# Optimization experiments

Hardware: AMD Instinct MI355X
Metric: run time of the kernel (lower is better)

## Reference

```python
import jax, jax.numpy as jnp
import numpy as np

N_NODES = 50000
N_EDGES = 800000
IN_DIM = 256
HID = 64          # per-head hidden dim
HEADS = 4
OUT_DIM = 64
NEG_SLOPE = 0.2


def setup_inputs() -> dict:
    key = jax.random.key(0)
    ks = jax.random.split(key, 10)
    x = jax.random.normal(ks[0], (N_NODES, IN_DIM), dtype=jnp.float32)
    src = jax.random.randint(ks[1], (N_EDGES,), 0, N_NODES, dtype=jnp.int32)
    dst = jax.random.randint(ks[2], (N_EDGES,), 0, N_NODES, dtype=jnp.int32)
    # layer 1: IN_DIM -> HEADS x HID (concat)
    W1 = jax.random.normal(ks[3], (IN_DIM, HEADS * HID), dtype=jnp.float32) * (1.0 / np.sqrt(IN_DIM))
    al1 = jax.random.normal(ks[4], (HEADS, HID), dtype=jnp.float32) * 0.1
    ar1 = jax.random.normal(ks[5], (HEADS, HID), dtype=jnp.float32) * 0.1
    W2 = jax.random.normal(ks[6], (HEADS * HID, 1 * OUT_DIM), dtype=jnp.float32) * (1.0 / np.sqrt(HEADS * HID))
    al2 = jax.random.normal(ks[7], (1, OUT_DIM), dtype=jnp.float32) * 0.1
    ar2 = jax.random.normal(ks[8], (1, OUT_DIM), dtype=jnp.float32) * 0.1
    return {"x": x, "src": src, "dst": dst, "W1": W1, "al1": al1, "ar1": ar1,
            "W2": W2, "al2": al2, "ar2": ar2}


def gat_layer(h, src, dst, W, al, ar):
    # h: [N, F_in]; W: [F_in, H*D]; al/ar: [H, D]
    H, D = al.shape
    feat = (h @ W).reshape(-1, H, D)                       # [N, H, D]
    el = jnp.einsum('nhd,hd->nh', feat, al)                # [N, H]
    er = jnp.einsum('nhd,hd->nh', feat, ar)                # [N, H]
    e = jax.nn.leaky_relu(el[src] + er[dst], negative_slope=NEG_SLOPE)  # [E, H]
    # softmax over incoming edges of each destination node
    m = jax.ops.segment_max(e, dst, num_segments=N_NODES)  # [N, H]
    w = jnp.exp(e - m[dst])                                # [E, H]
    s = jax.ops.segment_sum(w, dst, num_segments=N_NODES)  # [N, H]
    alpha = w / s[dst]                                     # [E, H]
    msg = feat[src] * alpha[:, :, None]                    # [E, H, D]
    out = jax.ops.segment_sum(msg, dst, num_segments=N_NODES)  # [N, H, D]
    return out


def reference(x, src, dst, W1, al1, ar1, W2, al2, ar2):
    # layer 1: concat heads + elu (dropout disabled: eval mode)
    h1 = gat_layer(x, src, dst, W1, al1, ar1)              # [N, HEADS, HID]
    h1 = jax.nn.elu(h1.reshape(N_NODES, HEADS * HID))      # [N, HEADS*HID]
    # output layer: single head, mean over heads (trivial for H=1)
    h2 = gat_layer(h1, src, dst, W2, al2, ar2)             # [N, 1, OUT_DIM]
    logits = h2.mean(axis=1)                               # [N, OUT_DIM]
    return logits
```

## Files before the change

kernel.cpp:

```cpp
#include <hip/hip_runtime.h>
#include <math.h>

#define NNODES 50000
#define NEDGES 800000
#define INDIM 256
#define HID 64
#define HEADS 4
#define OUTDIM 64
#define NEG_SLOPE 0.2f
#define NB ((NNODES + 1023) / 1024)
#define HB ((NEDGES + 255) / 256)
#define XB ((NNODES * (INDIM / 8) + 255) / 256)
#define WB ((256 * 256 + 256 * 64 + 255) / 256)

typedef __attribute__((ext_vector_type(4))) float f32x4;
typedef _Float16 __attribute__((ext_vector_type(8))) half8;


__global__ __launch_bounds__(256) void bsum_kernel(const int* __restrict__ deg,
                                                   int* __restrict__ bsums) {
    int b = blockIdx.x, t = threadIdx.x;
    int base = b * 1024 + t * 4;
    int s = 0;
    #pragma unroll
    for (int e = 0; e < 4; ++e) { int i = base + e; if (i < NNODES) s += deg[i]; }
    #pragma unroll
    for (int o = 32; o; o >>= 1) s += __shfl_xor(s, o);
    __shared__ int ws[4];
    int lane = t & 63, wid = t >> 6;
    if (lane == 0) ws[wid] = s;
    __syncthreads();
    if (t == 0) bsums[b] = ws[0] + ws[1] + ws[2] + ws[3];
}

__global__ __launch_bounds__(256) void scan_write_kernel(const int* __restrict__ deg,
                                                         const int* __restrict__ bsums,
                                                         int* __restrict__ offs) {
    int b = blockIdx.x, t = threadIdx.x;
    int lane = t & 63, wid = t >> 6;
    int bv = (lane < b) ? bsums[lane] : 0;
    #pragma unroll
    for (int o = 32; o; o >>= 1) bv += __shfl_xor(bv, o);
    int base = b * 1024 + t * 4;
    int v[4]; int tsum = 0;
    #pragma unroll
    for (int e = 0; e < 4; ++e) {
        int i = base + e;
        v[e] = (i < NNODES) ? deg[i] : 0;
        tsum += v[e];
    }
    int p = tsum;
    #pragma unroll
    for (int o = 1; o < 64; o <<= 1) { int u = __shfl_up(p, o); if (lane >= o) p += u; }
    __shared__ int ws[4];
    if (lane == 63) ws[wid] = p;
    __syncthreads();
    int woff = 0;
    for (int i = 0; i < wid; ++i) woff += ws[i];
    int run = bv + woff + p - tsum;
    #pragma unroll
    for (int e = 0; e < 4; ++e) {
        int i = base + e;
        if (i < NNODES) { offs[i] = run; run += v[e]; }
    }
    if (b == 0 && t == 0) offs[NNODES] = NEDGES;
}


__global__ __launch_bounds__(256) void prep_kernel(const int* __restrict__ dst,
                                                   int* __restrict__ deg,
                                                   int* __restrict__ rank,
                                                   const float* __restrict__ W1,
                                                   _Float16* __restrict__ W1t,
                                                   const float* __restrict__ W2,
                                                   _Float16* __restrict__ W2t,
                                                   const float* __restrict__ x,
                                                   _Float16* __restrict__ xh) {
    int b = blockIdx.x;
    if (b < HB) {
        int i = b * 256 + threadIdx.x;
        if (i < NEDGES) rank[i] = atomicAdd(&deg[dst[i]], 1);
    } else if (b < HB + XB) {
        int i = (b - HB) * 256 + threadIdx.x;
        if (i < NNODES * (INDIM / 8)) {
            const float4* xp = (const float4*)x;
            float4 f0 = xp[(size_t)i * 2];
            float4 f1 = xp[(size_t)i * 2 + 1];
            half8 v;
            v[0] = (_Float16)f0.x; v[1] = (_Float16)f0.y;
            v[2] = (_Float16)f0.z; v[3] = (_Float16)f0.w;
            v[4] = (_Float16)f1.x; v[5] = (_Float16)f1.y;
            v[6] = (_Float16)f1.z; v[7] = (_Float16)f1.w;
            ((half8*)xh)[i] = v;
        }
    } else {
        int idx = (b - HB - XB) * 256 + threadIdx.x;
        if (idx < 256 * 256) {
            int k = idx >> 8, n = idx & 255;
            W1t[n * 256 + k] = (_Float16)W1[idx];
        } else if (idx < 256 * 256 + 256 * 64) {
            int j = idx - 256 * 256;
            int k = j >> 6, n = j & 63;
            W2t[n * 256 + k] = (_Float16)W2[j];
        }
    }
}


template <int BM, int BN, int ELR>
__device__ __forceinline__ void gemm_body(
        const _Float16* __restrict__ Ah,
        const _Float16* __restrict__ Bt,
        _Float16* __restrict__ C,
        const float* __restrict__ al, const float* __restrict__ ar,
        float* __restrict__ el, float* __restrict__ er,
        int M, int N, int m0, int n0) {
    constexpr int K = 256;
    constexpr int NT = BN / 32;
    constexpr int TM = BM / 32;
    int t = threadIdx.x;
    int lane = t & 63, w = t >> 6;
    int wm = w >> 1, wn = w & 1;
    int lr = lane & 15, quad = lane >> 4;

    f32x4 acc[TM][NT];
    #pragma unroll
    for (int i = 0; i < TM; ++i)
        #pragma unroll
        for (int j = 0; j < NT; ++j) acc[i][j] = (f32x4){0.f, 0.f, 0.f, 0.f};

    int arow[TM];
    #pragma unroll
    for (int i = 0; i < TM; ++i) {
        int r = m0 + wm * (BM / 2) + i * 16 + lr;
        arow[i] = (r < M) ? r : (M - 1);
    }
    int brow[NT];
    #pragma unroll
    for (int j = 0; j < NT; ++j) brow[j] = n0 + wn * NT * 16 + j * 16 + lr;

    #pragma unroll
    for (int kk = 0; kk < K; kk += 32) {
        half8 a[TM], b[NT];
        #pragma unroll
        for (int i = 0; i < TM; ++i)
            a[i] = *(const half8*)(Ah + (size_t)arow[i] * K + kk + quad * 8);
        #pragma unroll
        for (int j = 0; j < NT; ++j)
            b[j] = *(const half8*)(Bt + (size_t)brow[j] * K + kk + quad * 8);
        #pragma unroll
        for (int i = 0; i < TM; ++i)
            #pragma unroll
            for (int j = 0; j < NT; ++j)
                acc[i][j] = __builtin_amdgcn_mfma_f32_16x16x32_f16(a[i], b[j], acc[i][j], 0, 0, 0);
    }
    #pragma unroll
    for (int i = 0; i < TM; ++i) {
        #pragma unroll
        for (int r = 0; r < 4; ++r) {
            int row = m0 + wm * (BM / 2) + i * 16 + quad * 4 + r;
            if (row < M) {
                #pragma unroll
                for (int j = 0; j < NT; ++j)
                    C[(size_t)row * N + n0 + wn * NT * 16 + j * 16 + lr] =
                        (_Float16)acc[i][j][r];
            }
        }
    }
    if constexpr (ELR == 1) {
        int h = n0 / 64 + wn;
        float alh[NT], arh[NT];
        #pragma unroll
        for (int j = 0; j < NT; ++j) {
            alh[j] = al[h * 64 + j * 16 + lr];
            arh[j] = ar[h * 64 + j * 16 + lr];
        }
        #pragma unroll
        for (int i = 0; i < TM; ++i) {
            #pragma unroll
            for (int r = 0; r < 4; ++r) {
                float pel = 0.f, per = 0.f;
                #pragma unroll
                for (int j = 0; j < NT; ++j) {
                    pel = fmaf(acc[i][j][r], alh[j], pel);
                    per = fmaf(acc[i][j][r], arh[j], per);
                }
                #pragma unroll
                for (int o = 1; o < 16; o <<= 1) {
                    pel += __shfl_xor(pel, o);
                    per += __shfl_xor(per, o);
                }
                if (lr == 0) {
                    int row = m0 + wm * (BM / 2) + i * 16 + quad * 4 + r;
                    if (row < M) {
                        el[(size_t)row * 4 + h] = pel;
                        er[(size_t)row * 4 + h] = per;
                    }
                }
            }
        }
    }
    if constexpr (ELR == 2) {
        __shared__ float elbuf[BM], erbuf[BM];
        float alv[NT], arv[NT];
        #pragma unroll
        for (int j = 0; j < NT; ++j) {
            alv[j] = al[wn * NT * 16 + j * 16 + lr];
            arv[j] = ar[wn * NT * 16 + j * 16 + lr];
        }
        float pel_s[TM][4], per_s[TM][4];
        #pragma unroll
        for (int i = 0; i < TM; ++i) {
            #pragma unroll
            for (int r = 0; r < 4; ++r) {
                float pel = 0.f, per = 0.f;
                #pragma unroll
                for (int j = 0; j < NT; ++j) {
                    pel = fmaf(acc[i][j][r], alv[j], pel);
                    per = fmaf(acc[i][j][r], arv[j], per);
                }
                #pragma unroll
                for (int o = 1; o < 16; o <<= 1) {
                    pel += __shfl_xor(pel, o);
                    per += __shfl_xor(per, o);
                }
                pel_s[i][r] = pel; per_s[i][r] = per;
            }
        }
        if (wn == 1 && lr == 0) {
            #pragma unroll
            for (int i = 0; i < TM; ++i)
                #pragma unroll
                for (int r = 0; r < 4; ++r) {
                    int rl = wm * (BM / 2) + i * 16 + quad * 4 + r;
                    elbuf[rl] = pel_s[i][r];
                    erbuf[rl] = per_s[i][r];
                }
        }
        __syncthreads();
        if (wn == 0 && lr == 0) {
            #pragma unroll
            for (int i = 0; i < TM; ++i)
                #pragma unroll
                for (int r = 0; r < 4; ++r) {
                    int rl = wm * (BM / 2) + i * 16 + quad * 4 + r;
                    int row = m0 + rl;
                    if (row < M) {
                        el[row] = pel_s[i][r] + elbuf[rl];
                        er[row] = per_s[i][r] + erbuf[rl];
                    }
                }
        }
    }
}


__global__ __launch_bounds__(256) void gemm1_scatter_kernel(
        const _Float16* __restrict__ Ah, const _Float16* __restrict__ Bt,
        _Float16* __restrict__ C,
        const float* __restrict__ al, const float* __restrict__ ar,
        float* __restrict__ el, float* __restrict__ er,
        int gemmBlocks,
        const int* __restrict__ src, const int* __restrict__ dst,
        const int* __restrict__ rank,
        const int* __restrict__ offs,
        int* __restrict__ ssorted) {
    int b = blockIdx.x;
    if (b < gemmBlocks) {
        int m0 = (b >> 1) * 64, n0 = (b & 1) * 128;
        gemm_body<64, 128, 1>(Ah, Bt, C, al, ar, el, er, NNODES, 256, m0, n0);
    } else {
        int i = (b - gemmBlocks) * 256 + threadIdx.x;
        if (i < NEDGES) {
            int d = dst[i];
            ssorted[offs[d] + rank[i]] = src[i];
        }
    }
}


template <int BM, int BN, int ELR>
__global__ __launch_bounds__(256) void gemm_f16_kernel(
        const _Float16* __restrict__ Ah, const _Float16* __restrict__ Bt,
        _Float16* __restrict__ C,
        const float* __restrict__ al, const float* __restrict__ ar,
        float* __restrict__ el, float* __restrict__ er,
        int M, int N) {
    int m0 = blockIdx.y * BM, n0 = blockIdx.x * BN;
    gemm_body<BM, BN, ELR>(Ah, Bt, C, al, ar, el, er, M, N, m0, n0);
}


__global__ __launch_bounds__(256) void spmm1_kernel(const _Float16* __restrict__ feat,
                                                    const float* __restrict__ el,
                                                    const float* __restrict__ er,
                                                    const int* __restrict__ offs,
                                                    const int* __restrict__ ssorted,
                                                    _Float16* __restrict__ h1) {
    int n = blockIdx.x * 4 + (threadIdx.x >> 6);
    if (n >= NNODES) return;
    int l = threadIdx.x & 63;
    int p2 = l >> 5;
    int q  = l & 31;
    int h  = q >> 3;
    int start = offs[n], end = offs[n + 1];
    int nst = (end - start + 1) >> 1;
    float ern = er[(size_t)n * 4 + h];
    const half8* f8 = (const half8*)feat;
    float acc[8];
    #pragma unroll
    for (int i = 0; i < 8; ++i) acc[i] = 0.f;
    float ws = 0.f;
    half8 z;
    #pragma unroll
    for (int i = 0; i < 8; ++i) z[i] = (_Float16)0;
    int sjB = 0, sjN = 0;
    float elA = 0.f, elB = 0.f;
    half8 fvA = z, fvB = z;
    if (nst > 0) {
        int x0 = start + p2;
        int sjA = ssorted[x0 < end ? x0 : start];
        if (nst > 1) {
            int x1 = start + 2 + p2;
            sjB = ssorted[x1 < end ? x1 : start];
        }
        elA = el[(size_t)sjA * 4 + h];
        fvA = f8[(size_t)sjA * 32 + q];
    }
    for (int js = 0; js < nst; ++js) {
        if (js + 1 < nst) {
            elB = el[(size_t)sjB * 4 + h];
            fvB = f8[(size_t)sjB * 32 + q];
        }
        if (js + 2 < nst) {
            int x = start + (js + 2) * 2 + p2;
            sjN = ssorted[x < end ? x : start];
        }
        bool vld = (start + js * 2 + p2) < end;
        float ev = elA + ern;
        ev = ev > 0.f ? ev : NEG_SLOPE * ev;
        float w = vld ? __expf(ev) : 0.f;
        ws += w;
        #pragma unroll
        for (int i = 0; i < 8; ++i) acc[i] = fmaf(w, (float)fvA[i], acc[i]);
        elA = elB; fvA = fvB; sjB = sjN;
    }
    ws += __shfl_xor(ws, 32);
    #pragma unroll
    for (int i = 0; i < 8; ++i) acc[i] += __shfl_xor(acc[i], 32);
    if (l < 32) {
        float inv = ws > 0.f ? 1.f / ws : 0.f;
        half8 hv;
        #pragma unroll
        for (int i = 0; i < 8; ++i) {
            float v = acc[i] * inv;
            v = v > 0.f ? v : __expf(v) - 1.f;
            hv[i] = (_Float16)v;
        }
        *(half8*)&h1[(size_t)n * 256 + q * 8] = hv;
    }
}


__global__ __launch_bounds__(256) void spmm2_kernel(const _Float16* __restrict__ feat,
                                                    const float* __restrict__ el,
                                                    const float* __restrict__ er,
                                                    const int* __restrict__ offs,
                                                    const int* __restrict__ ssorted,
                                                    float* __restrict__ out) {
    int n = blockIdx.x * 4 + (threadIdx.x >> 6);
    if (n >= NNODES) return;
    int l = threadIdx.x & 63;
    int e8 = l >> 3, li = l & 7;
    int start = offs[n], end = offs[n + 1];
    int nst = (end - start + 7) >> 3;
    float ern = er[n];
    const half8* f8 = (const half8*)feat;
    float acc[8];
    #pragma unroll
    for (int i = 0; i < 8; ++i) acc[i] = 0.f;
    float ws = 0.f;
    half8 z;
    #pragma unroll
    for (int i = 0; i < 8; ++i) z[i] = (_Float16)0;
    int sjB = 0, sjN = 0;
    float elA = 0.f, elB = 0.f;
    half8 fvA = z, fvB = z;
    if (nst > 0) {
        int x0 = start + e8;
        int sjA = ssorted[x0 < end ? x0 : start];
        if (nst > 1) {
            int x1 = start + 8 + e8;
            sjB = ssorted[x1 < end ? x1 : start];
        }
        elA = el[sjA];
        fvA = f8[(size_t)sjA * 8 + li];
    }
    for (int js = 0; js < nst; ++js) {
        if (js + 1 < nst) {
            elB = el[sjB];
            fvB = f8[(size_t)sjB * 8 + li];
        }
        if (js + 2 < nst) {
            int x = start + (js + 2) * 8 + e8;
            sjN = ssorted[x < end ? x : start];
        }
        bool vld = (start + js * 8 + e8) < end;
        float ev = elA + ern;
        ev = ev > 0.f ? ev : NEG_SLOPE * ev;
        float w = vld ? __expf(ev) : 0.f;
        ws += w;
        #pragma unroll
        for (int i = 0; i < 8; ++i) acc[i] = fmaf(w, (float)fvA[i], acc[i]);
        elA = elB; fvA = fvB; sjB = sjN;
    }
    #pragma unroll
    for (int o = 8; o < 64; o <<= 1) {
        ws += __shfl_xor(ws, o);
        #pragma unroll
        for (int i = 0; i < 8; ++i) acc[i] += __shfl_xor(acc[i], o);
    }
    if (e8 == 0) {
        float inv = ws > 0.f ? 1.f / ws : 0.f;
        float4 o0, o1;
        o0.x = acc[0] * inv; o0.y = acc[1] * inv;
        o0.z = acc[2] * inv; o0.w = acc[3] * inv;
        o1.x = acc[4] * inv; o1.y = acc[5] * inv;
        o1.z = acc[6] * inv; o1.w = acc[7] * inv;
        float4* op = (float4*)(out + (size_t)n * 64 + li * 8);
        op[0] = o0; op[1] = o1;
    }
}


extern "C" void kernel_launch(void* const* d_in, const int* in_sizes, int n_in,
                              void* d_out, int out_size, void* d_ws, size_t ws_size,
                              hipStream_t stream) {
    const float* x   = (const float*)d_in[0];
    const int*   src = (const int*)d_in[1];
    const int*   dst = (const int*)d_in[2];
    const float* W1  = (const float*)d_in[3];
    const float* al1 = (const float*)d_in[4];
    const float* ar1 = (const float*)d_in[5];
    const float* W2  = (const float*)d_in[6];
    const float* al2 = (const float*)d_in[7];
    const float* ar2 = (const float*)d_in[8];
    float* out = (float*)d_out;

    char* ws = (char*)d_ws;
    size_t off = 0;
    auto alloc = [&](size_t bytes) -> void* {
        void* p = ws + off;
        off += (bytes + 255) & ~(size_t)255;
        return p;
    };
    _Float16* feat1 = (_Float16*)alloc((size_t)NNODES * 256 * 2);
    _Float16* h1    = (_Float16*)alloc((size_t)NNODES * 256 * 2);
    _Float16* W1t   = (_Float16*)alloc((size_t)256 * 256 * 2);
    _Float16* W2t   = (_Float16*)alloc((size_t)64 * 256 * 2);
    float* el1    = (float*)alloc((size_t)NNODES * 4 * 4);
    float* er1    = (float*)alloc((size_t)NNODES * 4 * 4);
    float* el2    = (float*)alloc((size_t)NNODES * 4);
    float* er2    = (float*)alloc((size_t)NNODES * 4);
    int* deg      = (int*)alloc((size_t)NNODES * 4);
    int* rank     = (int*)alloc((size_t)NEDGES * 4);
    int* offs     = (int*)alloc((size_t)(NNODES + 1) * 4);
    int* bsums    = (int*)alloc((size_t)NB * 4);
    int* ssorted  = (int*)alloc((size_t)NEDGES * 4);
    _Float16* feat2 = feat1;
    _Float16* xh = h1;

    hipMemsetAsync(deg, 0, (size_t)NNODES * 4, stream);

    prep_kernel<<<HB + XB + WB, 256, 0, stream>>>(dst, deg, rank, W1, W1t, W2, W2t, x, xh);

    bsum_kernel<<<NB, 256, 0, stream>>>(deg, bsums);
    scan_write_kernel<<<NB, 256, 0, stream>>>(deg, bsums, offs);

    int gemmBlocks = ((NNODES + 63) / 64) * 2;
    gemm1_scatter_kernel<<<gemmBlocks + HB, 256, 0, stream>>>(
        xh, W1t, feat1, al1, ar1, el1, er1, gemmBlocks,
        src, dst, rank, offs, ssorted);

    spmm1_kernel<<<(NNODES + 3) / 4, 256, 0, stream>>>(
        feat1, el1, er1, offs, ssorted, h1);

    gemm_f16_kernel<64, 64, 2><<<dim3(1, (NNODES + 63) / 64), 256, 0, stream>>>(
        h1, W2t, feat2, al2, ar2, el2, er2, NNODES, 64);
    spmm2_kernel<<<(NNODES + 3) / 4, 256, 0, stream>>>(
        feat2, el2, er2, offs, ssorted, out);
}
```

Baseline: 301.3 us.

## Store layer-1 features head-major and split spmm1 per head

The first GEMM now writes features and attention logits in head-major layout ([H][N][64] and [H][N]). spmm1 launches one block group per head, so each wavefront handles a single head and processes 8 edges in parallel (8 lanes per 128-byte row) instead of 2 edges across all heads. The aim is more edge-level parallelism and memory-level parallelism for the gather on low-degree nodes, and compact per-head gathers that make better use of the cache. The cost is that each node's edge indices and offsets are read four times, and a deeper shuffle reduction is needed.

```diff
diff --git a/kernel.cpp b/kernel.cpp
--- a/kernel.cpp
+++ b/kernel.cpp
@@ -160,10 +160,18 @@
         for (int r = 0; r < 4; ++r) {
             int row = m0 + wm * (BM / 2) + i * 16 + quad * 4 + r;
             if (row < M) {
-                #pragma unroll
-                for (int j = 0; j < NT; ++j)
-                    C[(size_t)row * N + n0 + wn * NT * 16 + j * 16 + lr] =
-                        (_Float16)acc[i][j][r];
+                if constexpr (ELR == 1) {
+                    int h = n0 / 64 + wn;
+                    #pragma unroll
+                    for (int j = 0; j < NT; ++j)
+                        C[((size_t)h * M + row) * 64 + j * 16 + lr] =
+                            (_Float16)acc[i][j][r];
+                } else {
+                    #pragma unroll
+                    for (int j = 0; j < NT; ++j)
+                        C[(size_t)row * N + n0 + wn * NT * 16 + j * 16 + lr] =
+                            (_Float16)acc[i][j][r];
+                }
             }
         }
     }
@@ -193,8 +201,8 @@
                 if (lr == 0) {
                     int row = m0 + wm * (BM / 2) + i * 16 + quad * 4 + r;
                     if (row < M) {
-                        el[(size_t)row * 4 + h] = pel;
-                        er[(size_t)row * 4 + h] = per;
+                        el[(size_t)h * M + row] = pel;
+                        er[(size_t)h * M + row] = per;
                     }
                 }
             }
@@ -292,21 +300,22 @@
 
 
 __global__ __launch_bounds__(256) void spmm1_kernel(const _Float16* __restrict__ feat,
-                                                    const float* __restrict__ el,
-                                                    const float* __restrict__ er,
+                                                    const float* __restrict__ elh,
+                                                    const float* __restrict__ erh,
                                                     const int* __restrict__ offs,
                                                     const int* __restrict__ ssorted,
                                                     _Float16* __restrict__ h1) {
-    int n = blockIdx.x * 4 + (threadIdx.x >> 6);
-    if (n >= NNODES) return;
+    int bx = blockIdx.x;
+    int g = bx / (NNODES / 4);
+    int nc = bx - g * (NNODES / 4);
+    int n = nc * 4 + (threadIdx.x >> 6);
     int l = threadIdx.x & 63;
-    int p2 = l >> 5;
-    int q  = l & 31;
-    int h  = q >> 3;
+    int e8 = l >> 3, li = l & 7;
     int start = offs[n], end = offs[n + 1];
-    int nst = (end - start + 1) >> 1;
-    float ern = er[(size_t)n * 4 + h];
-    const half8* f8 = (const half8*)feat;
+    int nst = (end - start + 7) >> 3;
+    const float* el = elh + (size_t)g * NNODES;
+    float ern = erh[(size_t)g * NNODES + n];
+    const half8* f8 = (const half8*)feat + (size_t)g * NNODES * 8;
     float acc[8];
     #pragma unroll
     for (int i = 0; i < 8; ++i) acc[i] = 0.f;
@@ -318,25 +327,25 @@
     float elA = 0.f, elB = 0.f;
     half8 fvA = z, fvB = z;
     if (nst > 0) {
-        int x0 = start + p2;
+        int x0 = start + e8;
         int sjA = ssorted[x0 < end ? x0 : start];
         if (nst > 1) {
-            int x1 = start + 2 + p2;
+            int x1 = start + 8 + e8;
             sjB = ssorted[x1 < end ? x1 : start];
         }
-        elA = el[(size_t)sjA * 4 + h];
-        fvA = f8[(size_t)sjA * 32 + q];
+        elA = el[sjA];
+        fvA = f8[(size_t)sjA * 8 + li];
     }
     for (int js = 0; js < nst; ++js) {
         if (js + 1 < nst) {
-            elB = el[(size_t)sjB * 4 + h];
-            fvB = f8[(size_t)sjB * 32 + q];
+            elB = el[sjB];
+            fvB = f8[(size_t)sjB * 8 + li];
         }
         if (js + 2 < nst) {
-            int x = start + (js + 2) * 2 + p2;
+            int x = start + (js + 2) * 8 + e8;
             sjN = ssorted[x < end ? x : start];
         }
-        bool vld = (start + js * 2 + p2) < end;
+        bool vld = (start + js * 8 + e8) < end;
         float ev = elA + ern;
         ev = ev > 0.f ? ev : NEG_SLOPE * ev;
         float w = vld ? __expf(ev) : 0.f;
@@ -345,10 +354,13 @@
         for (int i = 0; i < 8; ++i) acc[i] = fmaf(w, (float)fvA[i], acc[i]);
         elA = elB; fvA = fvB; sjB = sjN;
     }
-    ws += __shfl_xor(ws, 32);
-    #pragma unroll
-    for (int i = 0; i < 8; ++i) acc[i] += __shfl_xor(acc[i], 32);
-    if (l < 32) {
+    #pragma unroll
+    for (int o = 8; o < 64; o <<= 1) {
+        ws += __shfl_xor(ws, o);
+        #pragma unroll
+        for (int i = 0; i < 8; ++i) acc[i] += __shfl_xor(acc[i], o);
+    }
+    if (e8 == 0) {
         float inv = ws > 0.f ? 1.f / ws : 0.f;
         half8 hv;
         #pragma unroll
@@ -357,7 +369,7 @@
             v = v > 0.f ? v : __expf(v) - 1.f;
             hv[i] = (_Float16)v;
         }
-        *(half8*)&h1[(size_t)n * 256 + q * 8] = hv;
+        *(half8*)&h1[(size_t)n * 256 + g * 64 + li * 8] = hv;
     }
 }
 
@@ -458,8 +470,8 @@
     _Float16* h1    = (_Float16*)alloc((size_t)NNODES * 256 * 2);
     _Float16* W1t   = (_Float16*)alloc((size_t)256 * 256 * 2);
     _Float16* W2t   = (_Float16*)alloc((size_t)64 * 256 * 2);
-    float* el1    = (float*)alloc((size_t)NNODES * 4 * 4);
-    float* er1    = (float*)alloc((size_t)NNODES * 4 * 4);
+    float* el1    = (float*)alloc((size_t)HEADS * NNODES * 4);
+    float* er1    = (float*)alloc((size_t)HEADS * NNODES * 4);
     float* el2    = (float*)alloc((size_t)NNODES * 4);
     float* er2    = (float*)alloc((size_t)NNODES * 4);
     int* deg      = (int*)alloc((size_t)NNODES * 4);
@@ -482,7 +494,7 @@
         xh, W1t, feat1, al1, ar1, el1, er1, gemmBlocks,
         src, dst, rank, offs, ssorted);
 
-    spmm1_kernel<<<(NNODES + 3) / 4, 256, 0, stream>>>(
+    spmm1_kernel<<<HEADS * (NNODES / 4), 256, 0, stream>>>(
         feat1, el1, er1, offs, ssorted, h1);
 
     gemm_f16_kernel<64, 64, 2><<<dim3(1, (NNODES + 63) / 64), 256, 0, stream>>>(
```

After: 317.7 us. 1.05x slower.
